# Optimization experiments

Hardware: AMD Instinct MI355X
Metric: run time of the kernel (lower is better)

Reference implementation:

```python
import jax, jax.numpy as jnp
import numpy as np
from jax import lax

WIN_SIZE = 11
BANDWIDTH = 0.5


def _regression(rand, target, win_size, bandwidth):
    """Sliding-window bandwidth-weighted regression moments.

    For each pixel p, over window neighbors q:
      w_pq = exp(-||target_p - target_q||^2 / bandwidth^2)   (guide-based kernel)
      x  = sum_q w * t_q / wgtSum
      xx = sum_q w * t_q^2 / wgtSum
      xy = sum_q w * t_q * r_q / wgtSum
      y  = sum_q w * r_q / wgtSum
    """
    B, H, W, C = target.shape
    R = win_size // 2
    inv_bw2 = 1.0 / (bandwidth * bandwidth)

    pad_cfg = ((0, 0), (R, R), (R, R), (0, 0))
    t_pad = jnp.pad(target, pad_cfg)
    r_pad = jnp.pad(rand, pad_cfg)
    # validity mask so out-of-image taps contribute zero weight
    m_pad = jnp.pad(jnp.ones((B, H, W, 1), dtype=target.dtype), pad_cfg)

    # all (dy, dx) offsets in the window, scanned sequentially (static count)
    offs = np.stack(np.meshgrid(np.arange(win_size), np.arange(win_size),
                                indexing='ij'), axis=-1).reshape(-1, 2)
    offs = jnp.asarray(offs, dtype=jnp.int32)

    zeros_c = jnp.zeros((B, H, W, C), dtype=target.dtype)
    zeros_1 = jnp.zeros((B, H, W, 1), dtype=target.dtype)

    def body(carry, off):
        x, xx, xy, y, wsum = carry
        dy, dx = off[0], off[1]
        t_s = lax.dynamic_slice(t_pad, (0, dy, dx, 0), (B, H, W, C))
        r_s = lax.dynamic_slice(r_pad, (0, dy, dx, 0), (B, H, W, C))
        m_s = lax.dynamic_slice(m_pad, (0, dy, dx, 0), (B, H, W, 1))
        # per-pixel squared color distance on the guide, summed over channels
        d = jnp.sum((target - t_s) ** 2, axis=-1, keepdims=True)  # [B,H,W,1]
        w = jnp.exp(-d * inv_bw2) * m_s                           # [B,H,W,1]
        return (x + w * t_s,
                xx + w * t_s * t_s,
                xy + w * t_s * r_s,
                y + w * r_s,
                wsum + w), None

    (x, xx, xy, y, wsum), _ = lax.scan(
        body, (zeros_c, zeros_c, zeros_c, zeros_c, zeros_1), offs)

    inv_w = 1.0 / wsum  # wsum >= 1 (center tap has w=1), safe
    return x * inv_w, xx * inv_w, xy * inv_w, y * inv_w


def setup_inputs() -> dict:
    key = jax.random.key(0)
    k1, k2 = jax.random.split(key)
    B, H, W, C = 4, 720, 1280, 3
    rand = jax.random.uniform(k1, (B, H, W, C), dtype=jnp.float32)
    target = jax.random.uniform(k2, (B, H, W, C), dtype=jnp.float32)
    return {"rand": rand, "target": target}


def reference(rand, target):
    return _regression(rand, target, WIN_SIZE, BANDWIDTH)
```

## Files before the change

kernel.cpp:

```cpp
#include <hip/hip_runtime.h>


#define HH   720
#define WW   1280
#define BB   4
#define RAD  5
#define TX   64
#define TY   16
#define KX   4
#define LH   26
#define LSTR 76
#define PLANE (LSTR * LH)
#define LDS_FLOATS 12288

__global__ __launch_bounds__(256, 3)
void regression_kernel(const float* __restrict__ rnd,
                       const float* __restrict__ tgt,
                       float* __restrict__ out)
{
    __shared__ __align__(16) float lds[LDS_FLOATS];
    float* pt0 = lds;
    float* pt1 = lds + PLANE;
    float* pt2 = lds + 2 * PLANE;
    float* pr0 = lds + 3 * PLANE;
    float* pr1 = lds + 4 * PLANE;
    float* pr2 = lds + 5 * PLANE;

    const int tx = threadIdx.x;
    const int ty = threadIdx.y;
    const int tid = ty * 16 + tx;
    const int X0 = blockIdx.x * TX;
    const int Y0 = blockIdx.y * TY;
    const int b  = blockIdx.z;

    const float SENT = 1e19f;

    for (int i = tid; i < PLANE; i += 256) {
        int ly = i / LSTR;
        int lx = i - ly * LSTR;
        int gy = Y0 + ly - RAD;
        int gx = X0 + lx - RAD;
        float t0 = SENT, t1 = SENT, t2 = SENT, r0 = 0.f, r1 = 0.f, r2 = 0.f;
        if ((unsigned)gy < (unsigned)HH && (unsigned)gx < (unsigned)WW) {
            int off = ((b * HH + gy) * WW + gx) * 3;
            t0 = tgt[off + 0]; t1 = tgt[off + 1]; t2 = tgt[off + 2];
            r0 = rnd[off + 0]; r1 = rnd[off + 1]; r2 = rnd[off + 2];
        }
        pt0[i] = t0; pt1[i] = t1; pt2[i] = t2;
        pr0[i] = r0; pr1[i] = r1; pr2[i] = r2;
    }
    __syncthreads();

    float tp0[KX], tp1[KX], tp2[KX];
    {
        int s = (ty + RAD) * LSTR + tx * KX + RAD;
        #pragma unroll
        for (int k = 0; k < KX; ++k) {
            tp0[k] = pt0[s + k]; tp1[k] = pt1[s + k]; tp2[k] = pt2[s + k];
        }
    }

    float sx0[KX] = {}, sx1[KX] = {}, sx2[KX] = {};
    float sxx0[KX] = {}, sxx1[KX] = {}, sxx2[KX] = {};
    float sxy0[KX] = {}, sxy1[KX] = {}, sxy2[KX] = {};
    float sy0[KX] = {}, sy1[KX] = {}, sy2[KX] = {};
    float sw[KX] = {};

    const float CC = -5.770780163555852f;

#define TAPK(k)                                                         \
    {                                                                   \
        float d0 = tp0[k] - t0;                                         \
        float d1 = tp1[k] - t1;                                         \
        float d2 = tp2[k] - t2;                                         \
        float d  = d0 * d0;                                             \
        d = fmaf(d1, d1, d);                                            \
        d = fmaf(d2, d2, d);                                            \
        float w = exp2f(d * CC);         \
        float wt0 = w * t0, wt1 = w * t1, wt2 = w * t2;                 \
        sx0[k] += wt0;  sx1[k] += wt1;  sx2[k] += wt2;                  \
        sxx0[k] = fmaf(wt0, t0, sxx0[k]);                               \
        sxx1[k] = fmaf(wt1, t1, sxx1[k]);                               \
        sxx2[k] = fmaf(wt2, t2, sxx2[k]);                               \
        sxy0[k] = fmaf(wt0, r0, sxy0[k]);                               \
        sxy1[k] = fmaf(wt1, r1, sxy1[k]);                               \
        sxy2[k] = fmaf(wt2, r2, sxy2[k]);                               \
        sy0[k]  = fmaf(w, r0, sy0[k]);                                  \
        sy1[k]  = fmaf(w, r1, sy1[k]);                                  \
        sy2[k]  = fmaf(w, r2, sy2[k]);                                  \
        sw[k]  += w;                                                    \
    }

    #pragma unroll 1
    for (int dy = 0; dy < 11; ++dy) {
        const int rb = (ty + dy) * LSTR + tx * KX;
        float T0[8], T1[8], T2[8], R0[8], R1[8], R2[8];

        *(float4*)&T0[0] = *(const float4*)(pt0 + rb);
        *(float4*)&T0[4] = *(const float4*)(pt0 + rb + 4);
        *(float4*)&T1[0] = *(const float4*)(pt1 + rb);
        *(float4*)&T1[4] = *(const float4*)(pt1 + rb + 4);
        *(float4*)&T2[0] = *(const float4*)(pt2 + rb);
        *(float4*)&T2[4] = *(const float4*)(pt2 + rb + 4);
        *(float4*)&R0[0] = *(const float4*)(pr0 + rb);
        *(float4*)&R0[4] = *(const float4*)(pr0 + rb + 4);
        *(float4*)&R1[0] = *(const float4*)(pr1 + rb);
        *(float4*)&R1[4] = *(const float4*)(pr1 + rb + 4);
        *(float4*)&R2[0] = *(const float4*)(pr2 + rb);
        *(float4*)&R2[4] = *(const float4*)(pr2 + rb + 4);

        #pragma unroll
        for (int j = 0; j < 8; ++j) {
            const float t0 = T0[j], t1 = T1[j], t2 = T2[j];
            const float r0 = R0[j], r1 = R1[j], r2 = R2[j];
            #pragma unroll
            for (int k = 0; k < KX; ++k)
                if (k <= j)
                    TAPK(k)
        }

        *(float4*)&T0[0] = *(const float4*)(pt0 + rb + 8);
        *(float4*)&T0[4] = *(const float4*)(pt0 + rb + 12);
        *(float4*)&T1[0] = *(const float4*)(pt1 + rb + 8);
        *(float4*)&T1[4] = *(const float4*)(pt1 + rb + 12);
        *(float4*)&T2[0] = *(const float4*)(pt2 + rb + 8);
        *(float4*)&T2[4] = *(const float4*)(pt2 + rb + 12);
        *(float4*)&R0[0] = *(const float4*)(pr0 + rb + 8);
        *(float4*)&R0[4] = *(const float4*)(pr0 + rb + 12);
        *(float4*)&R1[0] = *(const float4*)(pr1 + rb + 8);
        *(float4*)&R1[4] = *(const float4*)(pr1 + rb + 12);
        *(float4*)&R2[0] = *(const float4*)(pr2 + rb + 8);
        *(float4*)&R2[4] = *(const float4*)(pr2 + rb + 12);

        #pragma unroll
        for (int j2 = 0; j2 < 6; ++j2) {
            const float t0 = T0[j2], t1 = T1[j2], t2 = T2[j2];
            const float r0 = R0[j2], r1 = R1[j2], r2 = R2[j2];
            #pragma unroll
            for (int k = 0; k < KX; ++k)
                if (k >= j2 - 2)
                    TAPK(k)
        }
    }
#undef TAPK

    float inv[KX];
    #pragma unroll
    for (int k = 0; k < KX; ++k) inv[k] = 1.0f / sw[k];

    __syncthreads();

    float4* l4 = (float4*)lds;
    {
        const int b4 = ty * 48 + tx * 3;
#define STAGE_CHUNK(a0, a1, a2, cidx)                                          \
        {                                                                      \
            float4* p = l4 + (cidx) * 768 + b4;                                \
            p[0] = make_float4(a0[0]*inv[0], a1[0]*inv[0], a2[0]*inv[0],       \
                               a0[1]*inv[1]);                                  \
            p[1] = make_float4(a1[1]*inv[1], a2[1]*inv[1], a0[2]*inv[2],       \
                               a1[2]*inv[2]);                                  \
            p[2] = make_float4(a2[2]*inv[2], a0[3]*inv[3], a1[3]*inv[3],       \
                               a2[3]*inv[3]);                                  \
        }
        STAGE_CHUNK(sx0,  sx1,  sx2,  0)
        STAGE_CHUNK(sxx0, sxx1, sxx2, 1)
        STAGE_CHUNK(sxy0, sxy1, sxy2, 2)
        STAGE_CHUNK(sy0,  sy1,  sy2,  3)
#undef STAGE_CHUNK
    }
    __syncthreads();

    const int CH = BB * HH * WW * 3;
    int rr[3], cc4[3];
    #pragma unroll
    for (int m = 0; m < 3; ++m) {
        int r = m * 256 + tid;
        rr[m]  = r / 48;
        cc4[m] = r - rr[m] * 48;
    }
    #pragma unroll
    for (int i = 0; i < 12; ++i) {
        const int c = i / 3;
        const int m = i - c * 3;
        float4 v = l4[c * 768 + m * 256 + tid];
        const int gaddr = c * CH + ((b * HH + Y0 + rr[m]) * WW + X0) * 3 + cc4[m] * 4;
        *(float4*)(out + gaddr) = v;
    }
}

extern "C" void kernel_launch(void* const* d_in, const int* in_sizes, int n_in,
                              void* d_out, int out_size, void* d_ws, size_t ws_size,
                              hipStream_t stream) {
    const float* rnd = (const float*)d_in[0];
    const float* tgt = (const float*)d_in[1];
    float* out = (float*)d_out;

    dim3 grid(WW / TX, HH / TY, BB);
    dim3 block(16, 16);
    regression_kernel<<<grid, block, 0, stream>>>(rnd, tgt, out);
}
```

Baseline: 647.8 us.

## Halve per-thread column tile to two pixels and raise occupancy

Shrinks the block tile from 64 to 32 columns, so each thread accumulates 2 pixels instead of 4. This cuts register pressure and LDS footprint, and the launch bound is raised to target 6 blocks per CU. The LDS row loads become 12-wide float2 reads and the output staging and store loop are reworked to match. It also swaps exp2f for the raw hardware exp2 builtin. The trade-off is more halo reloading relative to useful work and less register reuse of loaded taps per pixel.

```diff
diff --git a/kernel.cpp b/kernel.cpp
--- a/kernel.cpp
+++ b/kernel.cpp
@@ -5,15 +5,16 @@
 #define WW   1280
 #define BB   4
 #define RAD  5
-#define TX   64
+#define TX   32
 #define TY   16
-#define KX   4
+#define KX   2
+#define LW   42
 #define LH   26
-#define LSTR 76
+#define LSTR 42
 #define PLANE (LSTR * LH)
-#define LDS_FLOATS 12288
+#define LDS_FLOATS (6 * PLANE)
 
-__global__ __launch_bounds__(256, 3)
+__global__ __launch_bounds__(256, 6)
 void regression_kernel(const float* __restrict__ rnd,
                        const float* __restrict__ tgt,
                        float* __restrict__ out)
@@ -76,7 +77,7 @@
         float d  = d0 * d0;                                             \
         d = fmaf(d1, d1, d);                                            \
         d = fmaf(d2, d2, d);                                            \
-        float w = exp2f(d * CC);         \
+        float w = __builtin_amdgcn_exp2f(d * CC);         \
         float wt0 = w * t0, wt1 = w * t1, wt2 = w * t2;                 \
         sx0[k] += wt0;  sx1[k] += wt1;  sx2[k] += wt2;                  \
         sxx0[k] = fmaf(wt0, t0, sxx0[k]);                               \
@@ -94,74 +95,40 @@
     #pragma unroll 1
     for (int dy = 0; dy < 11; ++dy) {
         const int rb = (ty + dy) * LSTR + tx * KX;
-        float T0[8], T1[8], T2[8], R0[8], R1[8], R2[8];
-
-        *(float4*)&T0[0] = *(const float4*)(pt0 + rb);
-        *(float4*)&T0[4] = *(const float4*)(pt0 + rb + 4);
-        *(float4*)&T1[0] = *(const float4*)(pt1 + rb);
-        *(float4*)&T1[4] = *(const float4*)(pt1 + rb + 4);
-        *(float4*)&T2[0] = *(const float4*)(pt2 + rb);
-        *(float4*)&T2[4] = *(const float4*)(pt2 + rb + 4);
-        *(float4*)&R0[0] = *(const float4*)(pr0 + rb);
-        *(float4*)&R0[4] = *(const float4*)(pr0 + rb + 4);
-        *(float4*)&R1[0] = *(const float4*)(pr1 + rb);
-        *(float4*)&R1[4] = *(const float4*)(pr1 + rb + 4);
-        *(float4*)&R2[0] = *(const float4*)(pr2 + rb);
-        *(float4*)&R2[4] = *(const float4*)(pr2 + rb + 4);
-
+        float T0[12], T1[12], T2[12], R0[12], R1[12], R2[12];
         #pragma unroll
-        for (int j = 0; j < 8; ++j) {
+        for (int m = 0; m < 6; ++m) {
+            *(float2*)&T0[2*m] = *(const float2*)(pt0 + rb + 2*m);
+            *(float2*)&T1[2*m] = *(const float2*)(pt1 + rb + 2*m);
+            *(float2*)&T2[2*m] = *(const float2*)(pt2 + rb + 2*m);
+            *(float2*)&R0[2*m] = *(const float2*)(pr0 + rb + 2*m);
+            *(float2*)&R1[2*m] = *(const float2*)(pr1 + rb + 2*m);
+            *(float2*)&R2[2*m] = *(const float2*)(pr2 + rb + 2*m);
+        }
+        #pragma unroll
+        for (int j = 0; j < 12; ++j) {
             const float t0 = T0[j], t1 = T1[j], t2 = T2[j];
             const float r0 = R0[j], r1 = R1[j], r2 = R2[j];
-            #pragma unroll
-            for (int k = 0; k < KX; ++k)
-                if (k <= j)
-                    TAPK(k)
-        }
-
-        *(float4*)&T0[0] = *(const float4*)(pt0 + rb + 8);
-        *(float4*)&T0[4] = *(const float4*)(pt0 + rb + 12);
-        *(float4*)&T1[0] = *(const float4*)(pt1 + rb + 8);
-        *(float4*)&T1[4] = *(const float4*)(pt1 + rb + 12);
-        *(float4*)&T2[0] = *(const float4*)(pt2 + rb + 8);
-        *(float4*)&T2[4] = *(const float4*)(pt2 + rb + 12);
-        *(float4*)&R0[0] = *(const float4*)(pr0 + rb + 8);
-        *(float4*)&R0[4] = *(const float4*)(pr0 + rb + 12);
-        *(float4*)&R1[0] = *(const float4*)(pr1 + rb + 8);
-        *(float4*)&R1[4] = *(const float4*)(pr1 + rb + 12);
-        *(float4*)&R2[0] = *(const float4*)(pr2 + rb + 8);
-        *(float4*)&R2[4] = *(const float4*)(pr2 + rb + 12);
-
-        #pragma unroll
-        for (int j2 = 0; j2 < 6; ++j2) {
-            const float t0 = T0[j2], t1 = T1[j2], t2 = T2[j2];
-            const float r0 = R0[j2], r1 = R1[j2], r2 = R2[j2];
-            #pragma unroll
-            for (int k = 0; k < KX; ++k)
-                if (k >= j2 - 2)
-                    TAPK(k)
+            if (j <= 10) TAPK(0)
+            if (j >= 1)  TAPK(1)
         }
     }
 #undef TAPK
 
-    float inv[KX];
-    #pragma unroll
-    for (int k = 0; k < KX; ++k) inv[k] = 1.0f / sw[k];
+    const float inv0 = 1.0f / sw[0];
+    const float inv1 = 1.0f / sw[1];
 
     __syncthreads();
 
-    float4* l4 = (float4*)lds;
+    float2* l2 = (float2*)lds;
     {
-        const int b4 = ty * 48 + tx * 3;
-#define STAGE_CHUNK(a0, a1, a2, cidx)                                          \
-        {                                                                      \
-            float4* p = l4 + (cidx) * 768 + b4;                                \
-            p[0] = make_float4(a0[0]*inv[0], a1[0]*inv[0], a2[0]*inv[0],       \
-                               a0[1]*inv[1]);                                  \
-            p[1] = make_float4(a1[1]*inv[1], a2[1]*inv[1], a0[2]*inv[2],       \
-                               a1[2]*inv[2]);                                  \
-            p[2] = make_float4(a2[2]*inv[2], a0[3]*inv[3], a1[3]*inv[3],       \
-                               a2[3]*inv[3]);                                  \
+        const int b2 = ty * 48 + tx * 3;
+#define STAGE_CHUNK(a0, a1, a2, cidx)                                   \
+        {                                                               \
+            float2* p = l2 + (cidx) * 768 + b2;                         \
+            p[0] = make_float2(a0[0]*inv0, a1[0]*inv0);                 \
+            p[1] = make_float2(a2[0]*inv0, a0[1]*inv1);                 \
+            p[2] = make_float2(a1[1]*inv1, a2[1]*inv1);                 \
         }
         STAGE_CHUNK(sx0,  sx1,  sx2,  0)
         STAGE_CHUNK(sxx0, sxx1, sxx2, 1)
@@ -172,19 +139,16 @@
     __syncthreads();
 
     const int CH = BB * HH * WW * 3;
-    int rr[3], cc4[3];
+    float4* l4 = (float4*)lds;
     #pragma unroll
-    for (int m = 0; m < 3; ++m) {
-        int r = m * 256 + tid;
-        rr[m]  = r / 48;
-        cc4[m] = r - rr[m] * 48;
-    }
-    #pragma unroll
-    for (int i = 0; i < 12; ++i) {
-        const int c = i / 3;
-        const int m = i - c * 3;
-        float4 v = l4[c * 768 + m * 256 + tid];
-        const int gaddr = c * CH + ((b * HH + Y0 + rr[m]) * WW + X0) * 3 + cc4[m] * 4;
+    for (int m = 0; m < 6; ++m) {
+        const int r = m * 256 + tid;
+        const int c = r / 384;
+        const int q = r - c * 384;
+        const int row = q / 24;
+        const int c4  = q - row * 24;
+        float4 v = l4[r];
+        const int gaddr = c * CH + ((b * HH + Y0 + row) * WW + X0) * 3 + c4 * 4;
         *(float4*)(out + gaddr) = v;
     }
 }
```

Result: slower. 2.496 ms (+285.3%).
